# Performance work log

Measured on AMD Instinct MI355X. Metric: run time of the kernel, lower is better.

Reference implementation:

```python
import jax, jax.numpy as jnp
import numpy as np

B, N, C = 16, 8192, 384   # batch, points, feature dim
G, M = 512, 32            # num_group (FPS centers), group_size (KNN k)


def setup_inputs() -> dict:
    key = jax.random.key(0)
    k1, k2 = jax.random.split(key)
    xyz = jax.random.normal(k1, (B, N, 3), dtype=jnp.float32)
    features = jax.random.normal(k2, (B, N, C), dtype=jnp.float32)
    return {"xyz": xyz, "features": features}


def _fps(xyz, n_samples):
    """Farthest point sampling, deterministic start at index 0 (matches CUDA op).
    xyz: [B, N, 3] -> idx: [B, n_samples] int32."""
    b, n, _ = xyz.shape
    big = jnp.asarray(1e10, xyz.dtype)

    def step(carry, _):
        min_dist, farthest = carry
        centroid = jnp.take_along_axis(xyz, farthest[:, None, None], axis=1)  # [B,1,3]
        d = jnp.sum((xyz - centroid) ** 2, axis=-1)                            # [B,N]
        min_dist = jnp.minimum(min_dist, d)
        nxt = jnp.argmax(min_dist, axis=-1).astype(jnp.int32)
        return (min_dist, nxt), farthest

    init = (jnp.full((b, n), big, xyz.dtype), jnp.zeros((b,), jnp.int32))
    _, idxs = jax.lax.scan(step, init, None, length=n_samples)  # [G, B]
    return jnp.transpose(idxs)  # [B, G]


def _knn_idx(ref, query, k):
    """Indices of k nearest ref points for each query. ref [B,N,3], query [B,G,3] -> [B,G,k]."""
    d = (jnp.sum(query ** 2, -1)[..., None]
         + jnp.sum(ref ** 2, -1)[:, None, :]
         - 2.0 * jnp.einsum('bgd,bnd->bgn', query, ref))  # [B,G,N]
    _, idx = jax.lax.top_k(-d, k)
    return idx


def reference(xyz, features):
    fps_idx = _fps(xyz, G)                                        # [B,G]
    center = jnp.take_along_axis(xyz, fps_idx[..., None], axis=1)  # [B,G,3]
    idx = _knn_idx(xyz, center, M)                                 # [B,G,M]

    gather = jax.vmap(lambda pts, i: pts[i])                       # per-batch fancy gather
    flat_idx = idx.reshape(B, G * M)
    neighborhood = gather(xyz, flat_idx).reshape(B, G, M, 3)
    feature_group = gather(features, flat_idx).reshape(B, G, M, C)
    neighborhood = neighborhood - center[:, :, None, :]
    return neighborhood, center, feature_group
```

## Files before the change

### kernel.cpp

```cpp
#include <hip/hip_runtime.h>
#include <math.h>

#define BATCH 16
#define NPTS  8192
#define FEATC 384
#define NG    512
#define KM    32

#define OUT0_OFF 0
#define OUT1_OFF (BATCH * NG * KM * 3)
#define OUT2_OFF (OUT1_OFF + BATCH * NG * 3)

#pragma clang fp contract(off)

typedef float f32x2 __attribute__((ext_vector_type(2)));
typedef float f32x4 __attribute__((ext_vector_type(4)));

template <int CTRL>
__device__ __forceinline__ int dpp1(int x) {
    return __builtin_amdgcn_update_dpp(x, x, CTRL, 0xF, 0xF, false);
}

__device__ __forceinline__ unsigned long long wave_max_u64(unsigned long long k) {
    unsigned long long o;
#define STEP(C)                                                                \
    {                                                                          \
        unsigned lo = (unsigned)dpp1<C>((int)(unsigned)k);                     \
        unsigned hi = (unsigned)dpp1<C>((int)(unsigned)(k >> 32));             \
        o = ((unsigned long long)hi << 32) | lo;                               \
        if (o > k) k = o;                                                      \
    }
    STEP(0x111) STEP(0x112) STEP(0x114) STEP(0x118) STEP(0x142) STEP(0x143)
#undef STEP
    return k;
}

__device__ __forceinline__ unsigned long long wave_min_u64(unsigned long long k) {
    unsigned long long o;
#define STEP(C)                                                                \
    {                                                                          \
        unsigned lo = (unsigned)dpp1<C>((int)(unsigned)k);                     \
        unsigned hi = (unsigned)dpp1<C>((int)(unsigned)(k >> 32));             \
        o = ((unsigned long long)hi << 32) | lo;                               \
        if (o < k) k = o;                                                      \
    }
    STEP(0x111) STEP(0x112) STEP(0x114) STEP(0x118) STEP(0x142) STEP(0x143)
#undef STEP
    return k;
}

__device__ __forceinline__ unsigned long long min16_u64(const unsigned long long* k) {
    unsigned long long t8[8];
#pragma unroll
    for (int i = 0; i < 8; ++i) t8[i] = k[i] < k[i + 8] ? k[i] : k[i + 8];
    unsigned long long t4[4];
#pragma unroll
    for (int i = 0; i < 4; ++i) t4[i] = t8[i] < t8[i + 4] ? t8[i] : t8[i + 4];
    unsigned long long a = t4[0] < t4[2] ? t4[0] : t4[2];
    unsigned long long b = t4[1] < t4[3] ? t4[1] : t4[3];
    return a < b ? a : b;
}

__global__ void init_progress(int* progress) {
    if (threadIdx.x < BATCH)
        __hip_atomic_store(&progress[threadIdx.x], 0,
                           __ATOMIC_RELAXED, __HIP_MEMORY_SCOPE_AGENT);
}

__global__ __launch_bounds__(512) void group_kernel(const float* __restrict__ xyz,
                                                    const float* __restrict__ features,
                                                    float* __restrict__ out0,
                                                    float* __restrict__ out1,
                                                    float* __restrict__ out2,
                                                    int* __restrict__ progress) {
#pragma clang fp contract(off)
    __shared__ unsigned long long sk[2][8];
    __shared__ int   sidx[KM];
    __shared__ float scst[24];

    const int tid  = threadIdx.x;
    const int lane = tid & 63;
    const int wid  = tid >> 6;

    if (blockIdx.x < BATCH) {
        const int b = blockIdx.x;
        const float* xb = xyz + (size_t)b * NPTS * 3;
        float* co = out1 + (size_t)b * NG * 3;
        const f32x4* cb = (const f32x4*)(xb + 48 * tid);

        f32x2 MD[8];
#pragma unroll
        for (int u = 0; u < 8; ++u) MD[u] = (f32x2){1e10f, 1e10f};

        int far = 0;
        for (int g = 0; g < NG; ++g) {
            f32x4 A0 = cb[0], A1 = cb[1], A2 = cb[2];
            f32x4 B0 = cb[3], B1 = cb[4], B2 = cb[5];

            const float cx = xb[far * 3 + 0];
            const float cy = xb[far * 3 + 1];
            const float cz = xb[far * 3 + 2];
            if (tid == 0) {
                scst[(g & 7) * 3 + 0] = cx;
                scst[(g & 7) * 3 + 1] = cy;
                scst[(g & 7) * 3 + 2] = cz;
            }
            const f32x2 cx2 = (f32x2){cx, cx};
            const f32x2 cy2 = (f32x2){cy, cy};
            const f32x2 cz2 = (f32x2){cz, cz};

#pragma unroll
            for (int c = 0; c < 4; ++c) {
                f32x2 xl = (f32x2){A0.x, A0.w};
                f32x2 yl = (f32x2){A0.y, A1.x};
                f32x2 zl = (f32x2){A0.z, A1.y};
                f32x2 xh = (f32x2){A1.z, A2.y};
                f32x2 yh = (f32x2){A1.w, A2.z};
                f32x2 zh = (f32x2){A2.x, A2.w};
                A0 = B0; A1 = B1; A2 = B2;
                if (c < 2) {
                    B0 = cb[3 * c + 6];
                    B1 = cb[3 * c + 7];
                    B2 = cb[3 * c + 8];
                }
                f32x2 dxl = xl - cx2, dyl = yl - cy2, dzl = zl - cz2;
                f32x2 dl  = (dxl * dxl + dyl * dyl) + dzl * dzl;
                MD[2 * c] = __builtin_elementwise_min(MD[2 * c], dl);
                f32x2 dxh = xh - cx2, dyh = yh - cy2, dzh = zh - cz2;
                f32x2 dh  = (dxh * dxh + dyh * dyh) + dzh * dzh;
                MD[2 * c + 1] = __builtin_elementwise_min(MD[2 * c + 1], dh);
            }

            f32x2 a0 = __builtin_elementwise_max(MD[0], MD[1]);
            f32x2 a1 = __builtin_elementwise_max(MD[2], MD[3]);
            f32x2 a2 = __builtin_elementwise_max(MD[4], MD[5]);
            f32x2 a3 = __builtin_elementwise_max(MD[6], MD[7]);
            f32x2 b0 = __builtin_elementwise_max(a0, a1);
            f32x2 b1 = __builtin_elementwise_max(a2, a3);
            f32x2 c0 = __builtin_elementwise_max(b0, b1);
            float lmax = fmaxf(c0.x, c0.y);

            unsigned cand = 0xFFFFFFFFu;
#pragma unroll
            for (int u = 7; u >= 0; --u) {
                if (MD[u].y == lmax) cand = (unsigned)(16 * tid + 2 * u + 1);
                if (MD[u].x == lmax) cand = (unsigned)(16 * tid + 2 * u);
            }

            unsigned long long key =
                ((unsigned long long)__float_as_uint(lmax) << 32) | (unsigned)(~cand);
            key = wave_max_u64(key);

            const int par = g & 1;
            if (lane == 63) sk[par][wid] = key;
            __syncthreads();

            unsigned long long m0 = sk[par][0] > sk[par][1] ? sk[par][0] : sk[par][1];
            unsigned long long m1 = sk[par][2] > sk[par][3] ? sk[par][2] : sk[par][3];
            unsigned long long m2 = sk[par][4] > sk[par][5] ? sk[par][4] : sk[par][5];
            unsigned long long m3 = sk[par][6] > sk[par][7] ? sk[par][6] : sk[par][7];
            unsigned long long ma = m0 > m1 ? m0 : m1;
            unsigned long long mb = m2 > m3 ? m2 : m3;
            unsigned long long gk = ma > mb ? ma : mb;
            far = (int)(~(unsigned)gk);

            if ((g & 7) == 7) {
                if (tid < 24) co[(g - 7) * 3 + tid] = scst[tid];
                if (tid == 0)
                    __hip_atomic_store(&progress[b], g + 1,
                                       __ATOMIC_RELEASE, __HIP_MEMORY_SCOPE_AGENT);
            }
        }
        return;
    }

    const int i = blockIdx.x - BATCH;
    const int b = i & 15;
    const int g = i >> 4;
    const int bgrow = b * NG + g;

    if (tid == 0) {
        while ((int)__hip_atomic_load(&progress[b], __ATOMIC_ACQUIRE,
                                      __HIP_MEMORY_SCOPE_AGENT) < g + 1)
            __builtin_amdgcn_s_sleep(127);
        unsigned* co = (unsigned*)out1 + (size_t)bgrow * 3;
        scst[0] = __uint_as_float(__hip_atomic_load(co + 0, __ATOMIC_RELAXED,
                                                    __HIP_MEMORY_SCOPE_AGENT));
        scst[1] = __uint_as_float(__hip_atomic_load(co + 1, __ATOMIC_RELAXED,
                                                    __HIP_MEMORY_SCOPE_AGENT));
        scst[2] = __uint_as_float(__hip_atomic_load(co + 2, __ATOMIC_RELAXED,
                                                    __HIP_MEMORY_SCOPE_AGENT));
    }
    __syncthreads();

    const float cx = scst[0], cy = scst[1], cz = scst[2];
    const float q2 = (cx * cx + cy * cy) + cz * cz;

    const float* xb = xyz + (size_t)b * NPTS * 3;

    unsigned long long k[16];
#pragma unroll
    for (int j = 0; j < 16; ++j) {
        int p = tid + (j << 9);
        float rx = xb[p * 3 + 0];
        float ry = xb[p * 3 + 1];
        float rz = xb[p * 3 + 2];
        float r2 = (rx * rx + ry * ry) + rz * rz;
        float dot = fmaf(cz, rz, fmaf(cy, ry, cx * rx));
        float d = (q2 + r2) - 2.0f * dot;
        unsigned u = __float_as_uint(d);
        u ^= ((unsigned)((int)u >> 31)) | 0x80000000u;
        k[j] = ((unsigned long long)u << 32) | (unsigned)p;
    }

    unsigned long long lv = min16_u64(k);
    unsigned long long wkey = wave_min_u64(lv);
    if (lane == 63) sk[0][wid] = wkey;
    __syncthreads();

    for (int kk = 0; kk < KM; ++kk) {
        const int par = kk & 1;
        const int nxt = par ^ 1;
        unsigned long long m0 = sk[par][0] < sk[par][1] ? sk[par][0] : sk[par][1];
        unsigned long long m1 = sk[par][2] < sk[par][3] ? sk[par][2] : sk[par][3];
        unsigned long long m2 = sk[par][4] < sk[par][5] ? sk[par][4] : sk[par][5];
        unsigned long long m3 = sk[par][6] < sk[par][7] ? sk[par][6] : sk[par][7];
        unsigned long long ma = m0 < m1 ? m0 : m1;
        unsigned long long mb = m2 < m3 ? m2 : m3;
        unsigned long long gk = ma < mb ? ma : mb;
        const unsigned pt = (unsigned)gk;
        const int wwave = (int)((pt & 511u) >> 6);

        if (wid == wwave) {
            if ((pt & 511u) == (unsigned)tid) {
                sidx[kk] = (int)pt;
                const unsigned jw = pt >> 9;
#pragma unroll
                for (int j = 0; j < 16; ++j) {
                    if ((unsigned)j == jw) k[j] = ~0ULL;
                }
                lv = min16_u64(k);
            }
            wkey = wave_min_u64(lv);
            if (lane == 63) sk[nxt][wid] = wkey;
        } else {
            if (lane == 63) sk[nxt][wid] = wkey;
        }
        __syncthreads();
    }

    if (tid < 96) {
        int m = tid / 3;
        int c = tid - 3 * m;
        int p = sidx[m];
        float v = xb[p * 3 + c] - scst[c];
        __builtin_nontemporal_store(v, &out0[((size_t)bgrow * KM + m) * 3 + c]);
    }

    const f32x4* fb = (const f32x4*)(features + (size_t)b * NPTS * FEATC);
    f32x4*       ob = (f32x4*)(out2 + (size_t)bgrow * KM * FEATC);
#pragma unroll
    for (int r = 0; r < 6; ++r) {
        int flat = tid + (r << 9);
        int m  = flat / 96;
        int c4 = flat - 96 * m;
        f32x4 v = __builtin_nontemporal_load(&fb[(size_t)sidx[m] * 96 + c4]);
        __builtin_nontemporal_store(v, &ob[(size_t)m * 96 + c4]);
    }
}

extern "C" void kernel_launch(void* const* d_in, const int* in_sizes, int n_in,
                              void* d_out, int out_size, void* d_ws, size_t ws_size,
                              hipStream_t stream) {
    const float* xyz      = (const float*)d_in[0];
    const float* features = (const float*)d_in[1];
    float* out  = (float*)d_out;
    float* out0 = out + OUT0_OFF;
    float* out1 = out + OUT1_OFF;
    float* out2 = out + OUT2_OFF;

    int* progress = (int*)d_ws;

    init_progress<<<1, 64, 0, stream>>>(progress);
    group_kernel<<<BATCH + BATCH * NG, 512, 0, stream>>>(xyz, features,
                                                         out0, out1, out2,
                                                         progress);
}
```

Baseline: 620.2 us.

## Use persistent consumer blocks with atomic work queue and keep them off FPS CUs

Replaces one block per (batch, group) KNN/gather task with a fixed pool of persistent consumer blocks that pull tasks from an atomic counter. Each FPS producer block records its CU id in a registry, and consumer blocks that land on the same CU exit so they do not compete with the serial FPS loop. FPS blocks also raise their wave priority. The aim is to stop consumers from stealing issue slots from the latency-critical FPS chain and to remove block launch overhead. In exchange it depends on hardware-register CU ids and on the consumer-to-CU placement leaving enough working blocks.

```diff
diff --git a/kernel.cpp b/kernel.cpp
--- a/kernel.cpp
+++ b/kernel.cpp
@@ -6,10 +6,16 @@
 #define FEATC 384
 #define NG    512
 #define KM    32
+#define NCONS 1008
 
 #define OUT0_OFF 0
 #define OUT1_OFF (BATCH * NG * KM * 3)
 #define OUT2_OFF (OUT1_OFF + BATCH * NG * 3)
+
+#define WS_INTS 34
+
+#define HWREG_HW_ID_FULL  ((31 << 11) | 4)
+#define HWREG_XCC_ID      ((3 << 11) | 20)
 
 #pragma clang fp contract(off)
 
@@ -61,9 +67,15 @@
     return a < b ? a : b;
 }
 
-__global__ void init_progress(int* progress) {
-    if (threadIdx.x < BATCH)
-        __hip_atomic_store(&progress[threadIdx.x], 0,
+__device__ __forceinline__ unsigned my_cu_key() {
+    unsigned hwid = (unsigned)__builtin_amdgcn_s_getreg(HWREG_HW_ID_FULL);
+    unsigned xcc  = (unsigned)__builtin_amdgcn_s_getreg(HWREG_XCC_ID);
+    return (xcc << 16) | (hwid & 0xFF00u) | 1u;
+}
+
+__global__ void init_ws(int* ws) {
+    if (threadIdx.x < WS_INTS)
+        __hip_atomic_store(&ws[threadIdx.x], 0,
                            __ATOMIC_RELAXED, __HIP_MEMORY_SCOPE_AGENT);
 }
 
@@ -72,11 +84,17 @@
                                                     float* __restrict__ out0,
                                                     float* __restrict__ out1,
                                                     float* __restrict__ out2,
-                                                    int* __restrict__ progress) {
+                                                    int* __restrict__ ws) {
 #pragma clang fp contract(off)
     __shared__ unsigned long long sk[2][8];
     __shared__ int   sidx[KM];
     __shared__ float scst[24];
+    __shared__ int   scom;
+
+    int* progress      = ws;
+    int* counter       = ws + 16;
+    int* regcount      = ws + 17;
+    unsigned* registry = (unsigned*)(ws + 18);
 
     const int tid  = threadIdx.x;
     const int lane = tid & 63;
@@ -84,6 +102,13 @@
 
     if (blockIdx.x < BATCH) {
         const int b = blockIdx.x;
+        if (tid == 0) {
+            __hip_atomic_store(&registry[b], my_cu_key(),
+                               __ATOMIC_RELAXED, __HIP_MEMORY_SCOPE_AGENT);
+            __hip_atomic_fetch_add(regcount, 1,
+                                   __ATOMIC_RELEASE, __HIP_MEMORY_SCOPE_AGENT);
+        }
+        __builtin_amdgcn_s_setprio(3);
         const float* xb = xyz + (size_t)b * NPTS * 3;
         float* co = out1 + (size_t)b * NG * 3;
         const f32x4* cb = (const f32x4*)(xb + 48 * tid);
@@ -174,98 +199,124 @@
         return;
     }
 
-    const int i = blockIdx.x - BATCH;
-    const int b = i & 15;
-    const int g = i >> 4;
-    const int bgrow = b * NG + g;
-
     if (tid == 0) {
-        while ((int)__hip_atomic_load(&progress[b], __ATOMIC_ACQUIRE,
-                                      __HIP_MEMORY_SCOPE_AGENT) < g + 1)
-            __builtin_amdgcn_s_sleep(127);
-        unsigned* co = (unsigned*)out1 + (size_t)bgrow * 3;
-        scst[0] = __uint_as_float(__hip_atomic_load(co + 0, __ATOMIC_RELAXED,
-                                                    __HIP_MEMORY_SCOPE_AGENT));
-        scst[1] = __uint_as_float(__hip_atomic_load(co + 1, __ATOMIC_RELAXED,
-                                                    __HIP_MEMORY_SCOPE_AGENT));
-        scst[2] = __uint_as_float(__hip_atomic_load(co + 2, __ATOMIC_RELAXED,
-                                                    __HIP_MEMORY_SCOPE_AGENT));
+        while ((int)__hip_atomic_load(regcount, __ATOMIC_ACQUIRE,
+                                      __HIP_MEMORY_SCOPE_AGENT) < BATCH)
+            __builtin_amdgcn_s_sleep(16);
+        unsigned mykey = my_cu_key();
+        int ex = 0;
+#pragma unroll
+        for (int i = 0; i < BATCH; ++i) {
+            unsigned rk = __hip_atomic_load(&registry[i], __ATOMIC_RELAXED,
+                                            __HIP_MEMORY_SCOPE_AGENT);
+            ex |= (rk == mykey);
+        }
+        scom = ex;
     }
     __syncthreads();
-
-    const float cx = scst[0], cy = scst[1], cz = scst[2];
-    const float q2 = (cx * cx + cy * cy) + cz * cz;
-
-    const float* xb = xyz + (size_t)b * NPTS * 3;
-
-    unsigned long long k[16];
-#pragma unroll
-    for (int j = 0; j < 16; ++j) {
-        int p = tid + (j << 9);
-        float rx = xb[p * 3 + 0];
-        float ry = xb[p * 3 + 1];
-        float rz = xb[p * 3 + 2];
-        float r2 = (rx * rx + ry * ry) + rz * rz;
-        float dot = fmaf(cz, rz, fmaf(cy, ry, cx * rx));
-        float d = (q2 + r2) - 2.0f * dot;
-        unsigned u = __float_as_uint(d);
-        u ^= ((unsigned)((int)u >> 31)) | 0x80000000u;
-        k[j] = ((unsigned long long)u << 32) | (unsigned)p;
-    }
-
-    unsigned long long lv = min16_u64(k);
-    unsigned long long wkey = wave_min_u64(lv);
-    if (lane == 63) sk[0][wid] = wkey;
-    __syncthreads();
-
-    for (int kk = 0; kk < KM; ++kk) {
-        const int par = kk & 1;
-        const int nxt = par ^ 1;
-        unsigned long long m0 = sk[par][0] < sk[par][1] ? sk[par][0] : sk[par][1];
-        unsigned long long m1 = sk[par][2] < sk[par][3] ? sk[par][2] : sk[par][3];
-        unsigned long long m2 = sk[par][4] < sk[par][5] ? sk[par][4] : sk[par][5];
-        unsigned long long m3 = sk[par][6] < sk[par][7] ? sk[par][6] : sk[par][7];
-        unsigned long long ma = m0 < m1 ? m0 : m1;
-        unsigned long long mb = m2 < m3 ? m2 : m3;
-        unsigned long long gk = ma < mb ? ma : mb;
-        const unsigned pt = (unsigned)gk;
-        const int wwave = (int)((pt & 511u) >> 6);
-
-        if (wid == wwave) {
-            if ((pt & 511u) == (unsigned)tid) {
-                sidx[kk] = (int)pt;
-                const unsigned jw = pt >> 9;
-#pragma unroll
-                for (int j = 0; j < 16; ++j) {
-                    if ((unsigned)j == jw) k[j] = ~0ULL;
+    if (scom) return;
+
+    for (;;) {
+        __syncthreads();
+        if (tid == 0) {
+            scom = __hip_atomic_fetch_add(counter, 1,
+                                          __ATOMIC_RELAXED, __HIP_MEMORY_SCOPE_AGENT);
+        }
+        __syncthreads();
+        const int n = scom;
+        if (n >= BATCH * NG) return;
+        const int b = n & 15;
+        const int g = n >> 4;
+        const int bgrow = b * NG + g;
+
+        if (tid == 0) {
+            while ((int)__hip_atomic_load(&progress[b], __ATOMIC_ACQUIRE,
+                                          __HIP_MEMORY_SCOPE_AGENT) < g + 1)
+                __builtin_amdgcn_s_sleep(127);
+            unsigned* co = (unsigned*)out1 + (size_t)bgrow * 3;
+            scst[0] = __uint_as_float(__hip_atomic_load(co + 0, __ATOMIC_RELAXED,
+                                                        __HIP_MEMORY_SCOPE_AGENT));
+            scst[1] = __uint_as_float(__hip_atomic_load(co + 1, __ATOMIC_RELAXED,
+                                                        __HIP_MEMORY_SCOPE_AGENT));
+            scst[2] = __uint_as_float(__hip_atomic_load(co + 2, __ATOMIC_RELAXED,
+                                                        __HIP_MEMORY_SCOPE_AGENT));
+        }
+        __syncthreads();
+
+        const float cx = scst[0], cy = scst[1], cz = scst[2];
+        const float q2 = (cx * cx + cy * cy) + cz * cz;
+
+        const float* xb = xyz + (size_t)b * NPTS * 3;
+
+        unsigned long long k[16];
+#pragma unroll
+        for (int j = 0; j < 16; ++j) {
+            int p = tid + (j << 9);
+            float rx = xb[p * 3 + 0];
+            float ry = xb[p * 3 + 1];
+            float rz = xb[p * 3 + 2];
+            float r2 = (rx * rx + ry * ry) + rz * rz;
+            float dot = fmaf(cz, rz, fmaf(cy, ry, cx * rx));
+            float d = (q2 + r2) - 2.0f * dot;
+            unsigned u = __float_as_uint(d);
+            u ^= ((unsigned)((int)u >> 31)) | 0x80000000u;
+            k[j] = ((unsigned long long)u << 32) | (unsigned)p;
+        }
+
+        unsigned long long lv = min16_u64(k);
+        unsigned long long wkey = wave_min_u64(lv);
+        if (lane == 63) sk[0][wid] = wkey;
+        __syncthreads();
+
+        for (int kk = 0; kk < KM; ++kk) {
+            const int par = kk & 1;
+            const int nxt = par ^ 1;
+            unsigned long long m0 = sk[par][0] < sk[par][1] ? sk[par][0] : sk[par][1];
+            unsigned long long m1 = sk[par][2] < sk[par][3] ? sk[par][2] : sk[par][3];
+            unsigned long long m2 = sk[par][4] < sk[par][5] ? sk[par][4] : sk[par][5];
+            unsigned long long m3 = sk[par][6] < sk[par][7] ? sk[par][6] : sk[par][7];
+            unsigned long long ma = m0 < m1 ? m0 : m1;
+            unsigned long long mb = m2 < m3 ? m2 : m3;
+            unsigned long long gk = ma < mb ? ma : mb;
+            const unsigned pt = (unsigned)gk;
+            const int wwave = (int)((pt & 511u) >> 6);
+
+            if (wid == wwave) {
+                if ((pt & 511u) == (unsigned)tid) {
+                    sidx[kk] = (int)pt;
+                    const unsigned jw = pt >> 9;
+#pragma unroll
+                    for (int j = 0; j < 16; ++j) {
+                        if ((unsigned)j == jw) k[j] = ~0ULL;
+                    }
+                    lv = min16_u64(k);
                 }
-                lv = min16_u64(k);
-            }
-            wkey = wave_min_u64(lv);
-            if (lane == 63) sk[nxt][wid] = wkey;
-        } else {
-            if (lane == 63) sk[nxt][wid] = wkey;
-        }
-        __syncthreads();
-    }
-
-    if (tid < 96) {
-        int m = tid / 3;
-        int c = tid - 3 * m;
-        int p = sidx[m];
-        float v = xb[p * 3 + c] - scst[c];
-        __builtin_nontemporal_store(v, &out0[((size_t)bgrow * KM + m) * 3 + c]);
-    }
-
-    const f32x4* fb = (const f32x4*)(features + (size_t)b * NPTS * FEATC);
-    f32x4*       ob = (f32x4*)(out2 + (size_t)bgrow * KM * FEATC);
-#pragma unroll
-    for (int r = 0; r < 6; ++r) {
-        int flat = tid + (r << 9);
-        int m  = flat / 96;
-        int c4 = flat - 96 * m;
-        f32x4 v = __builtin_nontemporal_load(&fb[(size_t)sidx[m] * 96 + c4]);
-        __builtin_nontemporal_store(v, &ob[(size_t)m * 96 + c4]);
+                wkey = wave_min_u64(lv);
+                if (lane == 63) sk[nxt][wid] = wkey;
+            } else {
+                if (lane == 63) sk[nxt][wid] = wkey;
+            }
+            __syncthreads();
+        }
+
+        if (tid < 96) {
+            int m = tid / 3;
+            int c = tid - 3 * m;
+            int p = sidx[m];
+            float v = xb[p * 3 + c] - scst[c];
+            __builtin_nontemporal_store(v, &out0[((size_t)bgrow * KM + m) * 3 + c]);
+        }
+
+        const f32x4* fb = (const f32x4*)(features + (size_t)b * NPTS * FEATC);
+        f32x4*       ob = (f32x4*)(out2 + (size_t)bgrow * KM * FEATC);
+#pragma unroll
+        for (int r = 0; r < 6; ++r) {
+            int flat = tid + (r << 9);
+            int m  = flat / 96;
+            int c4 = flat - 96 * m;
+            f32x4 v = __builtin_nontemporal_load(&fb[(size_t)sidx[m] * 96 + c4]);
+            __builtin_nontemporal_store(v, &ob[(size_t)m * 96 + c4]);
+        }
     }
 }
 
@@ -279,10 +330,9 @@
     float* out1 = out + OUT1_OFF;
     float* out2 = out + OUT2_OFF;
 
-    int* progress = (int*)d_ws;
-
-    init_progress<<<1, 64, 0, stream>>>(progress);
-    group_kernel<<<BATCH + BATCH * NG, 512, 0, stream>>>(xyz, features,
-                                                         out0, out1, out2,
-                                                         progress);
-}
+    int* ws = (int*)d_ws;
+
+    init_ws<<<1, 64, 0, stream>>>(ws);
+    group_kernel<<<BATCH + NCONS, 512, 0, stream>>>(xyz, features,
+                                                    out0, out1, out2, ws);
+}
```

After: 1.033 ms. 66.6% more time.
